# Kernel optimization log

Hardware: AMD Instinct MI355X
Metric: run time of the kernel (lower is better)

The kernel has to match this reference:

```python
import jax, jax.numpy as jnp
import numpy as np

N_NODES = 50000
N_EDGES = 500000
IN_DIM = 64
OUT_DIM = 64
NUM_RELS = 16


def setup_inputs() -> dict:
    key = jax.random.key(0)
    ks = jax.random.split(key, 8)
    h = jax.random.normal(ks[0], (N_NODES, IN_DIM), dtype=jnp.float32)
    he = jax.random.normal(ks[1], (N_EDGES, IN_DIM), dtype=jnp.float32)
    src = jax.random.randint(ks[2], (N_EDGES,), 0, N_NODES)
    dst = jax.random.randint(ks[3], (N_EDGES,), 0, N_NODES)
    rel = jax.random.randint(ks[4], (N_EDGES,), 0, NUM_RELS)
    # xavier-ish scales
    W_shared = jax.random.normal(ks[5], (OUT_DIM, IN_DIM), dtype=jnp.float32) * (2.0 / (IN_DIM + OUT_DIM)) ** 0.5
    W_attn = jax.random.normal(ks[6], (1, 3 * OUT_DIM), dtype=jnp.float32) * (2.0 / (3 * OUT_DIM + 1)) ** 0.5
    W_rel = jax.random.normal(ks[7], (NUM_RELS, IN_DIM, OUT_DIM), dtype=jnp.float32) * (2.0 / (IN_DIM + OUT_DIM)) ** 0.5
    return {"h": h, "he": he, "src": src, "dst": dst, "rel": rel,
            "W_shared": W_shared, "W_attn": W_attn, "W_rel": W_rel}


def reference(h, he, src, dst, rel, W_shared, W_attn, W_rel):
    # --- edge attention: a = attn_fc([z_src, z_edge, z_dst]) (raw linear score, no softmax in original) ---
    Z = h @ W_shared.T                      # [N, out] project all nodes once
    ze = he @ W_shared.T                    # [E, out]
    # split attn weight to avoid materializing [E, 3*out] concat
    Wa_s, Wa_e, Wa_d = jnp.split(W_attn, 3, axis=1)   # each [1, out]
    a = Z[src] @ Wa_s.T + ze @ Wa_e.T + Z[dst] @ Wa_d.T   # [E, 1]
    # --- message: msg = (h_src @ W_rel[rel]) * a ---
    # compute per-(node, relation) transform once [N, R, out], then gather per edge
    H_all = jnp.einsum('ni,rio->nro', h, W_rel)          # [N, R, out]
    msg = H_all[src, rel] * a                             # [E, out]
    # --- scatter-sum aggregation into destination nodes ---
    out = jax.ops.segment_sum(msg, dst, num_segments=N_NODES)  # [N, out]
    # apply_func: activation (relu), no bias
    return jax.nn.relu(out)
```

## Files before the change

### kernel.cpp

```cpp
#include <hip/hip_runtime.h>
#include <math.h>

#define N_NODES 50000
#define N_EDGES 500000
#define NUM_RELS 16
#define GH 64
#define SCAN_BLKS 196
#define AE_BLKS 1954

typedef _Float16 f16x8 __attribute__((ext_vector_type(8)));
typedef _Float16 f16x4 __attribute__((ext_vector_type(4)));
typedef float    f32x4 __attribute__((ext_vector_type(4)));


__global__ void kz(int* __restrict__ w) {
    int i = blockIdx.x * 256 + threadIdx.x;
    if (i < 5120) w[i] = 0;
    if (i < 1600000) w[100000 + i] = 0;
}

__global__ __launch_bounds__(256) void k_node(
    const float* __restrict__ h,
    const float* __restrict__ W_shared, const float* __restrict__ W_attn,
    const int* __restrict__ dst, const int* __restrict__ rel,
    float* __restrict__ sn, float* __restrict__ dn,
    int* __restrict__ c1, int* __restrict__ c2p,
    _Float16* __restrict__ h_hi, _Float16* __restrict__ h_lo) {
    __shared__ float sus[64], sud[64];
    __shared__ int hist[NUM_RELS];
    const int t = threadIdx.x, bid = blockIdx.x, nb = gridDim.x;
    if (t < 64) {
        float us = 0.f, ud = 0.f;
        for (int o = 0; o < 64; ++o) {
            float w = W_shared[o * 64 + t];
            us = fmaf(w, W_attn[o],       us);
            ud = fmaf(w, W_attn[128 + o], ud);
        }
        sus[t] = us; sud[t] = ud;
    }
    if (t < NUM_RELS) hist[t] = 0;
    __syncthreads();

    int n = bid * 256 + t;
    if (n < N_NODES) {
        const float* hp = h + (size_t)n * 64;
        float s = 0.f, d = 0.f;
#pragma unroll
        for (int i = 0; i < 64; i += 4) {
            float4 v = *(const float4*)(hp + i);
            s = fmaf(v.x, sus[i], s);     s = fmaf(v.y, sus[i + 1], s);
            s = fmaf(v.z, sus[i + 2], s); s = fmaf(v.w, sus[i + 3], s);
            d = fmaf(v.x, sud[i], d);     d = fmaf(v.y, sud[i + 1], d);
            d = fmaf(v.z, sud[i + 2], d); d = fmaf(v.w, sud[i + 3], d);
            f16x4 hi, lo;
            hi[0] = (_Float16)v.x; lo[0] = (_Float16)(v.x - (float)hi[0]);
            hi[1] = (_Float16)v.y; lo[1] = (_Float16)(v.y - (float)hi[1]);
            hi[2] = (_Float16)v.z; lo[2] = (_Float16)(v.z - (float)hi[2]);
            hi[3] = (_Float16)v.w; lo[3] = (_Float16)(v.w - (float)hi[3]);
            *(f16x4*)(h_hi + (size_t)n * 64 + i) = hi;
            *(f16x4*)(h_lo + (size_t)n * 64 + i) = lo;
        }
        sn[n] = s; dn[n] = d;
    }
    for (int e = bid * 256 + t; e < N_EDGES; e += nb * 256) {
        atomicAdd(&hist[rel[e]], 1);
        atomicAdd(&c2p[dst[e] << 4], 1);
    }
    __syncthreads();
    if (t < NUM_RELS && hist[t]) atomicAdd(&c1[t], hist[t]);
}

__global__ __launch_bounds__(256) void k_scan1(const int* __restrict__ c2p,
                                               int* __restrict__ partial) {
    const int t = threadIdx.x, bid = blockIdx.x;
    const int lane = t & 63, wv = t >> 6;
    __shared__ int ws[4];
    int idx = bid * 256 + t;
    int s = (idx < N_NODES) ? c2p[idx << 4] : 0;
#pragma unroll
    for (int off = 32; off > 0; off >>= 1) s += __shfl_xor(s, off, 64);
    if (lane == 0) ws[wv] = s;
    __syncthreads();
    if (t == 0) partial[bid] = ws[0] + ws[1] + ws[2] + ws[3];
}

__global__ __launch_bounds__(256) void k_scan2(const int* __restrict__ partial,
                                               int* __restrict__ pbase,
                                               int* __restrict__ offs2,
                                               const int* __restrict__ c1,
                                               int* __restrict__ offs1) {
    const int t = threadIdx.x;
    const int lane = t & 63, wv = t >> 6;
    __shared__ int wsum[4];
    int v = (t < SCAN_BLKS) ? partial[t] : 0;
    int x = v;
#pragma unroll
    for (int off = 1; off < 64; off <<= 1) {
        int y = __shfl_up(x, off, 64);
        if (lane >= off) x += y;
    }
    if (lane == 63) wsum[wv] = x;
    __syncthreads();
    int wbase = 0;
#pragma unroll
    for (int j = 0; j < 4; ++j) if (j < wv) wbase += wsum[j];
    int excl = wbase + x - v;
    pbase[t] = excl;
    if (t == 255) offs2[N_NODES] = excl;
    if (t == 0) {
        int b = 0;
        for (int r = 0; r < NUM_RELS; ++r) { offs1[r] = b; b += c1[r]; }
        offs1[NUM_RELS] = b;
    }
}

__global__ __launch_bounds__(256) void k_scan3(const int* __restrict__ c2p,
                                               const int* __restrict__ pbase,
                                               int* __restrict__ offs2) {
    const int t = threadIdx.x, bid = blockIdx.x;
    const int lane = t & 63, wv = t >> 6;
    __shared__ int wsum[4];
    int idx = bid * 256 + t;
    int v = (idx < N_NODES) ? c2p[idx << 4] : 0;
    int x = v;
#pragma unroll
    for (int off = 1; off < 64; off <<= 1) {
        int y = __shfl_up(x, off, 64);
        if (lane >= off) x += y;
    }
    if (lane == 63) wsum[wv] = x;
    __syncthreads();
    int wbase = 0;
#pragma unroll
    for (int j = 0; j < 4; ++j) if (j < wv) wbase += wsum[j];
    if (idx < N_NODES) offs2[idx] = pbase[bid] + wbase + x - v;
}

__global__ __launch_bounds__(256) void k_ae(
    const float4* __restrict__ he4,
    const int* __restrict__ src, const int* __restrict__ dst,
    const int* __restrict__ rel,
    const float* __restrict__ W_shared, const float* __restrict__ W_attn,
    const float* __restrict__ sn, const float* __restrict__ dn,
    const int* __restrict__ offs1, int* __restrict__ cur1p,
    const int* __restrict__ offs2, int* __restrict__ cur2p,
    int* __restrict__ srcs, float* __restrict__ aes, int* __restrict__ iperm) {
    __shared__ float sve[64];
    __shared__ float sdot[256];
    __shared__ int hist[NUM_RELS], bbase[NUM_RELS], soffs[NUM_RELS];
    const int t = threadIdx.x;
    const int lane = t & 63;
    const int w = t >> 6;
    const int e = blockIdx.x * 256 + t;

    const size_t fb = ((size_t)blockIdx.x * 256 + (size_t)w * 64) * 16;
    const size_t fmax = (size_t)N_EDGES * 16 - 1;
    float4 v[16];
#pragma unroll
    for (int k = 0; k < 16; ++k) {
        size_t fi = fb + (size_t)k * 64 + lane;
        if (fi > fmax) fi = fmax;
        v[k] = he4[fi];
    }

    if (t < 64) {
        float ve = 0.f;
        for (int o = 0; o < 64; ++o)
            ve = fmaf(W_shared[o * 64 + t], W_attn[64 + o], ve);
        sve[t] = ve;
    }
    if (t < NUM_RELS) { hist[t] = 0; soffs[t] = offs1[t]; }
    const bool valid = (e < N_EDGES);
    int r = 0, s_ = 0, d_ = 0;
    float sdv = 0.f;
    if (valid) {
        s_ = src[e]; d_ = dst[e]; r = rel[e];
        sdv = sn[s_] + dn[d_];
    }
    __syncthreads();

    {
        float4 u = *(const float4*)(sve + 4 * (lane & 15));
#pragma unroll
        for (int k = 0; k < 16; ++k) {
            float p = v[k].x * u.x + v[k].y * u.y + v[k].z * u.z + v[k].w * u.w;
            p += __shfl_xor(p, 1, 64);
            p += __shfl_xor(p, 2, 64);
            p += __shfl_xor(p, 4, 64);
            p += __shfl_xor(p, 8, 64);
            if ((lane & 15) == 0) sdot[w * 64 + k * 4 + (lane >> 4)] = p;
        }
    }
    int lpos = 0; float aev = 0.f;
    if (valid) {
        aev = sdot[t] + sdv;
        lpos = atomicAdd(&hist[r], 1);
    }
    __syncthreads();
    if (t < NUM_RELS) bbase[t] = hist[t] ? atomicAdd(&cur1p[t << 8], hist[t]) : 0;
    __syncthreads();
    if (valid) {
        int p1 = soffs[r] + bbase[r] + lpos;
        srcs[p1] = s_; aes[p1] = aev;
        int p2 = offs2[d_] + atomicAdd(&cur2p[d_ << 4], 1);
        iperm[p2] = p1;
    }
}

__global__ __launch_bounds__(256, 4) void k_msg(
    const _Float16* __restrict__ h_hi, const _Float16* __restrict__ h_lo,
    const float* __restrict__ W_rel, const int* __restrict__ offs1,
    const int* __restrict__ srcs, const float* __restrict__ aes,
    float* __restrict__ msg)
{
    const int t = threadIdx.x;
    const int lane = t & 63;
    const int quad = lane >> 4;
    const int col  = lane & 15;
    const int wib  = t >> 6;
    const int rh   = blockIdx.x & 31;
    const int r    = rh & 15;
    const int half = rh >> 4;
    const int g    = blockIdx.x >> 5;
    const int wr   = g * 4 + wib;

    const int begin = __builtin_amdgcn_readfirstlane(offs1[r]);
    const int end   = __builtin_amdgcn_readfirstlane(offs1[r + 1]);

    const float* Wb = W_rel + (size_t)r * 4096;
    f16x8 bh[2][2], bl[2][2];
#pragma unroll
    for (int kb = 0; kb < 2; ++kb)
#pragma unroll
        for (int n2 = 0; n2 < 2; ++n2)
#pragma unroll
            for (int j = 0; j < 8; ++j) {
                float w = Wb[(kb * 32 + quad * 8 + j) * 64 + (half * 2 + n2) * 16 + col];
                _Float16 hi = (_Float16)w;
                bh[kb][n2][j] = hi;
                bl[kb][n2][j] = (_Float16)(w - (float)hi);
            }

    for (int base = begin + wr * 16; base < end; base += 256 * 16) {
        int m16 = end - base; if (m16 > 16) m16 = 16;
        const int ridx = base + (col < m16 ? col : m16 - 1);
        const int   sv = srcs[ridx];
        const float av = (col < m16) ? aes[ridx] : 0.f;

        const _Float16* ph = h_hi + (size_t)sv * 64 + quad * 8;
        const _Float16* pl = h_lo + (size_t)sv * 64 + quad * 8;
        f16x8 ah0 = *(const f16x8*)ph, ah1 = *(const f16x8*)(ph + 32);
        f16x8 al0 = *(const f16x8*)pl, al1 = *(const f16x8*)(pl + 32);

        f32x4 acc0 = {0.f, 0.f, 0.f, 0.f};
        f32x4 acc1 = {0.f, 0.f, 0.f, 0.f};
        acc0 = __builtin_amdgcn_mfma_f32_16x16x32_f16(ah0, bh[0][0], acc0, 0, 0, 0);
        acc1 = __builtin_amdgcn_mfma_f32_16x16x32_f16(ah0, bh[0][1], acc1, 0, 0, 0);
        acc0 = __builtin_amdgcn_mfma_f32_16x16x32_f16(ah0, bl[0][0], acc0, 0, 0, 0);
        acc1 = __builtin_amdgcn_mfma_f32_16x16x32_f16(ah0, bl[0][1], acc1, 0, 0, 0);
        acc0 = __builtin_amdgcn_mfma_f32_16x16x32_f16(al0, bh[0][0], acc0, 0, 0, 0);
        acc1 = __builtin_amdgcn_mfma_f32_16x16x32_f16(al0, bh[0][1], acc1, 0, 0, 0);
        acc0 = __builtin_amdgcn_mfma_f32_16x16x32_f16(ah1, bh[1][0], acc0, 0, 0, 0);
        acc1 = __builtin_amdgcn_mfma_f32_16x16x32_f16(ah1, bh[1][1], acc1, 0, 0, 0);
        acc0 = __builtin_amdgcn_mfma_f32_16x16x32_f16(ah1, bl[1][0], acc0, 0, 0, 0);
        acc1 = __builtin_amdgcn_mfma_f32_16x16x32_f16(ah1, bl[1][1], acc1, 0, 0, 0);
        acc0 = __builtin_amdgcn_mfma_f32_16x16x32_f16(al1, bh[1][0], acc0, 0, 0, 0);
        acc1 = __builtin_amdgcn_mfma_f32_16x16x32_f16(al1, bh[1][1], acc1, 0, 0, 0);

#pragma unroll
        for (int reg = 0; reg < 4; ++reg) {
            const int m = quad * 4 + reg;
            const float am = __shfl(av, m, 64);
            if (m < m16) {
                float* op = msg + (size_t)(base + m) * 64 + half * 32 + col;
                op[0]  = am * acc0[reg];
                op[16] = am * acc1[reg];
            }
        }
    }
}

__global__ __launch_bounds__(256) void k_out(
    const float* __restrict__ msg, const int* __restrict__ iperm,
    const int* __restrict__ offs2, float* __restrict__ out)
{
    const int lane = threadIdx.x & 63;
    const int gw   = blockIdx.x * 4 + (threadIdx.x >> 6);
    const int nw   = gridDim.x * 4;
    for (int n = gw; n < N_NODES; n += nw) {
        const int qb = offs2[n], qe = offs2[n + 1];
        float s0 = 0.f, s1 = 0.f, s2 = 0.f, s3 = 0.f;
        float s4 = 0.f, s5 = 0.f, s6 = 0.f, s7 = 0.f;
        int q = qb;
        for (; q + 8 <= qe; q += 8) {
            int p0 = iperm[q],     p1 = iperm[q + 1];
            int p2 = iperm[q + 2], p3 = iperm[q + 3];
            int p4 = iperm[q + 4], p5 = iperm[q + 5];
            int p6 = iperm[q + 6], p7 = iperm[q + 7];
            s0 += msg[(size_t)p0 * 64 + lane];
            s1 += msg[(size_t)p1 * 64 + lane];
            s2 += msg[(size_t)p2 * 64 + lane];
            s3 += msg[(size_t)p3 * 64 + lane];
            s4 += msg[(size_t)p4 * 64 + lane];
            s5 += msg[(size_t)p5 * 64 + lane];
            s6 += msg[(size_t)p6 * 64 + lane];
            s7 += msg[(size_t)p7 * 64 + lane];
        }
        for (; q + 2 <= qe; q += 2) {
            int p0 = iperm[q], p1 = iperm[q + 1];
            s0 += msg[(size_t)p0 * 64 + lane];
            s1 += msg[(size_t)p1 * 64 + lane];
        }
        if (q < qe)
            s0 += msg[(size_t)iperm[q] * 64 + lane];
        float s = ((s0 + s1) + (s2 + s3)) + ((s4 + s5) + (s6 + s7));
        out[(size_t)n * 64 + lane] = fmaxf(s, 0.f);
    }
}

extern "C" void kernel_launch(void* const* d_in, const int* in_sizes, int n_in,
                              void* d_out, int out_size, void* d_ws, size_t ws_size,
                              hipStream_t stream) {
    const float*  h        = (const float*)d_in[0];
    const float4* he4      = (const float4*)d_in[1];
    const int*    src      = (const int*)d_in[2];
    const int*    dst      = (const int*)d_in[3];
    const int*    rel      = (const int*)d_in[4];
    const float*  W_shared = (const float*)d_in[5];
    const float*  W_attn   = (const float*)d_in[6];
    const float*  W_rel    = (const float*)d_in[7];
    float*        out      = (float*)d_out;

    int*      c1      = (int*)d_ws + 0;
    int*      cur1p   = (int*)d_ws + 1024;
    int*      offs1   = (int*)d_ws + 5200;
    int*      c2p     = (int*)d_ws + 100000;
    int*      cur2p   = (int*)d_ws + 900000;
    int*      offs2   = (int*)d_ws + 1700000;
    float*    sn      = (float*)d_ws + 1760000;
    float*    dn      = (float*)d_ws + 1810000;
    int*      srcs    = (int*)d_ws + 1860000;
    float*    aes     = (float*)d_ws + 2360000;
    int*      iperm   = (int*)d_ws + 2860000;
    _Float16* h_hi    = (_Float16*)((int*)d_ws + 3360000);
    _Float16* h_lo    = (_Float16*)((int*)d_ws + 4960000);
    int*      partial = srcs;
    int*      pbase   = srcs + 256;
    float*    msg     = (float*)d_in[1];

    kz<<<6250, 256, 0, stream>>>((int*)d_ws);
    k_node<<<196, 256, 0, stream>>>(h, W_shared, W_attn, dst, rel,
                                    sn, dn, c1, c2p, h_hi, h_lo);
    k_scan1<<<SCAN_BLKS, 256, 0, stream>>>(c2p, partial);
    k_scan2<<<1, 256, 0, stream>>>(partial, pbase, offs2, c1, offs1);
    k_scan3<<<SCAN_BLKS, 256, 0, stream>>>(c2p, pbase, offs2);
    k_ae<<<AE_BLKS, 256, 0, stream>>>(he4, src, dst, rel, W_shared, W_attn, sn, dn,
                                      offs1, cur1p, offs2, cur2p, srcs, aes, iperm);
    k_msg<<<32 * GH, 256, 0, stream>>>(h_hi, h_lo, W_rel, offs1, srcs, aes, msg);
    k_out<<<2048, 256, 0, stream>>>(msg, iperm, offs2, out);
}
```

Baseline: 342.4 us.

## Move edge-feature attention dot into node/histogram pre-pass via async LDS loads

The edge-feature attention dot product (he · W_shared^T · Wa_e) moves out of k_ae into the first node/histogram kernel, now launched over the full edge grid. It stages he rows into LDS with global_load_lds and an XOR swizzle, and writes a per-edge scalar edot. k_ae then reads one float per edge instead of 256 bytes of he, so that kernel's load shortens and the he read overlaps with histogramming. In exchange the pre-pass uses 64 KB of dynamic shared memory per block, which limits occupancy, and adds a 2 MB edot round trip.

```diff
diff --git a/kernel.cpp b/kernel.cpp
--- a/kernel.cpp
+++ b/kernel.cpp
@@ -6,7 +6,7 @@
 #define NUM_RELS 16
 #define GH 64
 #define SCAN_BLKS 196
-#define AE_BLKS 1954
+#define PRE_BLKS 1954
 
 typedef _Float16 f16x8 __attribute__((ext_vector_type(8)));
 typedef _Float16 f16x4 __attribute__((ext_vector_type(4)));
@@ -19,52 +19,98 @@
     if (i < 1600000) w[100000 + i] = 0;
 }
 
-__global__ __launch_bounds__(256) void k_node(
-    const float* __restrict__ h,
+__global__ __launch_bounds__(256, 2) void k_pre(
+    const float* __restrict__ h, const char* __restrict__ heb,
     const float* __restrict__ W_shared, const float* __restrict__ W_attn,
     const int* __restrict__ dst, const int* __restrict__ rel,
     float* __restrict__ sn, float* __restrict__ dn,
     int* __restrict__ c1, int* __restrict__ c2p,
-    _Float16* __restrict__ h_hi, _Float16* __restrict__ h_lo) {
-    __shared__ float sus[64], sud[64];
+    _Float16* __restrict__ h_hi, _Float16* __restrict__ h_lo,
+    float* __restrict__ edot) {
+    extern __shared__ float stage[];
+    __shared__ float sus[64], sud[64], sve[64];
     __shared__ int hist[NUM_RELS];
-    const int t = threadIdx.x, bid = blockIdx.x, nb = gridDim.x;
+    const int t = threadIdx.x, bid = blockIdx.x;
+    const int l = t & 63, w = t >> 6;
+    const int e = bid * 256 + t;
+    const bool valid = (e < N_EDGES);
+
+    if (t < NUM_RELS) hist[t] = 0;
+
+    {
+        char* sb = (char*)stage + w * 16384;
+#pragma unroll
+        for (int k = 0; k < 16; ++k) {
+            const int u  = k * 64 + l;
+            const int tl = u >> 4;
+            const int j  = (u & 15) ^ (tl & 15);
+            int row = bid * 256 + w * 64 + tl;
+            if (row >= N_EDGES) row = N_EDGES - 1;
+            __builtin_amdgcn_global_load_lds(
+                (const void*)(heb + (size_t)row * 256 + (size_t)j * 16),
+                (void*)(sb + k * 1024), 16, 0, 0);
+        }
+    }
+
+    int dv = 0, rv = 0;
+    if (valid) { dv = dst[e]; rv = rel[e]; }
+
     if (t < 64) {
-        float us = 0.f, ud = 0.f;
+        float us = 0.f, ud = 0.f, ve = 0.f;
         for (int o = 0; o < 64; ++o) {
-            float w = W_shared[o * 64 + t];
-            us = fmaf(w, W_attn[o],       us);
-            ud = fmaf(w, W_attn[128 + o], ud);
-        }
-        sus[t] = us; sud[t] = ud;
-    }
-    if (t < NUM_RELS) hist[t] = 0;
+            float ww = W_shared[o * 64 + t];
+            us = fmaf(ww, W_attn[o],       us);
+            ve = fmaf(ww, W_attn[64 + o],  ve);
+            ud = fmaf(ww, W_attn[128 + o], ud);
+        }
+        sus[t] = us; sud[t] = ud; sve[t] = ve;
+    }
     __syncthreads();
 
     int n = bid * 256 + t;
-    if (n < N_NODES) {
+    if (bid < SCAN_BLKS && n < N_NODES) {
         const float* hp = h + (size_t)n * 64;
         float s = 0.f, d = 0.f;
 #pragma unroll
         for (int i = 0; i < 64; i += 4) {
-            float4 v = *(const float4*)(hp + i);
-            s = fmaf(v.x, sus[i], s);     s = fmaf(v.y, sus[i + 1], s);
-            s = fmaf(v.z, sus[i + 2], s); s = fmaf(v.w, sus[i + 3], s);
-            d = fmaf(v.x, sud[i], d);     d = fmaf(v.y, sud[i + 1], d);
-            d = fmaf(v.z, sud[i + 2], d); d = fmaf(v.w, sud[i + 3], d);
+            float4 hv = *(const float4*)(hp + i);
+            s = fmaf(hv.x, sus[i], s);     s = fmaf(hv.y, sus[i + 1], s);
+            s = fmaf(hv.z, sus[i + 2], s); s = fmaf(hv.w, sus[i + 3], s);
+            d = fmaf(hv.x, sud[i], d);     d = fmaf(hv.y, sud[i + 1], d);
+            d = fmaf(hv.z, sud[i + 2], d); d = fmaf(hv.w, sud[i + 3], d);
             f16x4 hi, lo;
-            hi[0] = (_Float16)v.x; lo[0] = (_Float16)(v.x - (float)hi[0]);
-            hi[1] = (_Float16)v.y; lo[1] = (_Float16)(v.y - (float)hi[1]);
-            hi[2] = (_Float16)v.z; lo[2] = (_Float16)(v.z - (float)hi[2]);
-            hi[3] = (_Float16)v.w; lo[3] = (_Float16)(v.w - (float)hi[3]);
+            hi[0] = (_Float16)hv.x; lo[0] = (_Float16)(hv.x - (float)hi[0]);
+            hi[1] = (_Float16)hv.y; lo[1] = (_Float16)(hv.y - (float)hi[1]);
+            hi[2] = (_Float16)hv.z; lo[2] = (_Float16)(hv.z - (float)hi[2]);
+            hi[3] = (_Float16)hv.w; lo[3] = (_Float16)(hv.w - (float)hi[3]);
             *(f16x4*)(h_hi + (size_t)n * 64 + i) = hi;
             *(f16x4*)(h_lo + (size_t)n * 64 + i) = lo;
         }
         sn[n] = s; dn[n] = d;
     }
-    for (int e = bid * 256 + t; e < N_EDGES; e += nb * 256) {
-        atomicAdd(&hist[rel[e]], 1);
-        atomicAdd(&c2p[dst[e] << 4], 1);
+
+    if (valid) {
+        atomicAdd(&hist[rv], 1);
+        atomicAdd(&c2p[dv << 4], 1);
+        const float4* sp = (const float4*)stage;
+        const int tx = t & 15;
+        float a0 = 0.f, a1 = 0.f, a2 = 0.f, a3 = 0.f;
+#pragma unroll
+        for (int i = 0; i < 16; i += 4) {
+            float4 v0 = sp[(t << 4) + ((i + 0) ^ tx)];
+            float4 u0 = *(const float4*)(sve + 4 * (i + 0));
+            float4 v1 = sp[(t << 4) + ((i + 1) ^ tx)];
+            float4 u1 = *(const float4*)(sve + 4 * (i + 1));
+            float4 v2 = sp[(t << 4) + ((i + 2) ^ tx)];
+            float4 u2 = *(const float4*)(sve + 4 * (i + 2));
+            float4 v3 = sp[(t << 4) + ((i + 3) ^ tx)];
+            float4 u3 = *(const float4*)(sve + 4 * (i + 3));
+            a0 += v0.x * u0.x + v0.y * u0.y + v0.z * u0.z + v0.w * u0.w;
+            a1 += v1.x * u1.x + v1.y * u1.y + v1.z * u1.z + v1.w * u1.w;
+            a2 += v2.x * u2.x + v2.y * u2.y + v2.z * u2.z + v2.w * u2.w;
+            a3 += v3.x * u3.x + v3.y * u3.y + v3.z * u3.z + v3.w * u3.w;
+        }
+        edot[e] = (a0 + a1) + (a2 + a3);
     }
     __syncthreads();
     if (t < NUM_RELS && hist[t]) atomicAdd(&c1[t], hist[t]);
@@ -137,65 +183,26 @@
 }
 
 __global__ __launch_bounds__(256) void k_ae(
-    const float4* __restrict__ he4,
     const int* __restrict__ src, const int* __restrict__ dst,
-    const int* __restrict__ rel,
-    const float* __restrict__ W_shared, const float* __restrict__ W_attn,
+    const int* __restrict__ rel, const float* __restrict__ edot,
     const float* __restrict__ sn, const float* __restrict__ dn,
     const int* __restrict__ offs1, int* __restrict__ cur1p,
     const int* __restrict__ offs2, int* __restrict__ cur2p,
     int* __restrict__ srcs, float* __restrict__ aes, int* __restrict__ iperm) {
-    __shared__ float sve[64];
-    __shared__ float sdot[256];
     __shared__ int hist[NUM_RELS], bbase[NUM_RELS], soffs[NUM_RELS];
     const int t = threadIdx.x;
-    const int lane = t & 63;
-    const int w = t >> 6;
     const int e = blockIdx.x * 256 + t;
-
-    const size_t fb = ((size_t)blockIdx.x * 256 + (size_t)w * 64) * 16;
-    const size_t fmax = (size_t)N_EDGES * 16 - 1;
-    float4 v[16];
-#pragma unroll
-    for (int k = 0; k < 16; ++k) {
-        size_t fi = fb + (size_t)k * 64 + lane;
-        if (fi > fmax) fi = fmax;
-        v[k] = he4[fi];
-    }
-
-    if (t < 64) {
-        float ve = 0.f;
-        for (int o = 0; o < 64; ++o)
-            ve = fmaf(W_shared[o * 64 + t], W_attn[64 + o], ve);
-        sve[t] = ve;
-    }
     if (t < NUM_RELS) { hist[t] = 0; soffs[t] = offs1[t]; }
     const bool valid = (e < N_EDGES);
     int r = 0, s_ = 0, d_ = 0;
-    float sdv = 0.f;
+    float aev = 0.f;
     if (valid) {
         s_ = src[e]; d_ = dst[e]; r = rel[e];
-        sdv = sn[s_] + dn[d_];
-    }
-    __syncthreads();
-
-    {
-        float4 u = *(const float4*)(sve + 4 * (lane & 15));
-#pragma unroll
-        for (int k = 0; k < 16; ++k) {
-            float p = v[k].x * u.x + v[k].y * u.y + v[k].z * u.z + v[k].w * u.w;
-            p += __shfl_xor(p, 1, 64);
-            p += __shfl_xor(p, 2, 64);
-            p += __shfl_xor(p, 4, 64);
-            p += __shfl_xor(p, 8, 64);
-            if ((lane & 15) == 0) sdot[w * 64 + k * 4 + (lane >> 4)] = p;
-        }
-    }
-    int lpos = 0; float aev = 0.f;
-    if (valid) {
-        aev = sdot[t] + sdv;
-        lpos = atomicAdd(&hist[r], 1);
-    }
+        aev = edot[e] + sn[s_] + dn[d_];
+    }
+    __syncthreads();
+    int lpos = 0;
+    if (valid) lpos = atomicAdd(&hist[r], 1);
     __syncthreads();
     if (t < NUM_RELS) bbase[t] = hist[t] ? atomicAdd(&cur1p[t << 8], hist[t]) : 0;
     __syncthreads();
@@ -322,7 +329,7 @@
                               void* d_out, int out_size, void* d_ws, size_t ws_size,
                               hipStream_t stream) {
     const float*  h        = (const float*)d_in[0];
-    const float4* he4      = (const float4*)d_in[1];
+    const char*   heb      = (const char*)d_in[1];
     const int*    src      = (const int*)d_in[2];
     const int*    dst      = (const int*)d_in[3];
     const int*    rel      = (const int*)d_in[4];
@@ -344,18 +351,19 @@
     int*      iperm   = (int*)d_ws + 2860000;
     _Float16* h_hi    = (_Float16*)((int*)d_ws + 3360000);
     _Float16* h_lo    = (_Float16*)((int*)d_ws + 4960000);
+    float*    edot    = (float*)d_ws + 6600000;
     int*      partial = srcs;
     int*      pbase   = srcs + 256;
     float*    msg     = (float*)d_in[1];
 
     kz<<<6250, 256, 0, stream>>>((int*)d_ws);
-    k_node<<<196, 256, 0, stream>>>(h, W_shared, W_attn, dst, rel,
-                                    sn, dn, c1, c2p, h_hi, h_lo);
+    k_pre<<<PRE_BLKS, 256, 65536, stream>>>(h, heb, W_shared, W_attn, dst, rel,
+                                            sn, dn, c1, c2p, h_hi, h_lo, edot);
     k_scan1<<<SCAN_BLKS, 256, 0, stream>>>(c2p, partial);
     k_scan2<<<1, 256, 0, stream>>>(partial, pbase, offs2, c1, offs1);
     k_scan3<<<SCAN_BLKS, 256, 0, stream>>>(c2p, pbase, offs2);
-    k_ae<<<AE_BLKS, 256, 0, stream>>>(he4, src, dst, rel, W_shared, W_attn, sn, dn,
-                                      offs1, cur1p, offs2, cur2p, srcs, aes, iperm);
+    k_ae<<<PRE_BLKS, 256, 0, stream>>>(src, dst, rel, edot, sn, dn,
+                                       offs1, cur1p, offs2, cur2p, srcs, aes, iperm);
     k_msg<<<32 * GH, 256, 0, stream>>>(h_hi, h_lo, W_rel, offs1, srcs, aes, msg);
     k_out<<<2048, 256, 0, stream>>>(msg, iperm, offs2, out);
 }
```

New measurement: 340.8 us. About the same (-0.5%).
